# Optimization experiments

Hardware: AMD Instinct MI355X
Metric: run time of the kernel (lower is better)

Reference implementation:

```python
import jax, jax.numpy as jnp
from jax import lax
import numpy as np

NUM_TAGS = 96
BATCH = 512
SEQ = 512


def setup_inputs() -> dict:
    key = jax.random.key(0)
    k1, k2, k3, k4, k5 = jax.random.split(key, 5)
    logits = jax.random.normal(k1, (BATCH, SEQ, NUM_TAGS), dtype=jnp.float32)
    tags = jax.random.randint(k2, (BATCH, SEQ), 0, NUM_TAGS, dtype=jnp.int64)
    mask = jnp.ones((BATCH, SEQ), dtype=jnp.int32)
    # learned CRF params, init U(-0.1, 0.1) as in reset_parameters()
    transitions = jax.random.uniform(k3, (NUM_TAGS, NUM_TAGS), minval=-0.1, maxval=0.1, dtype=jnp.float32)
    start_transitions = jax.random.uniform(k4, (NUM_TAGS,), minval=-0.1, maxval=0.1, dtype=jnp.float32)
    end_transitions = jax.random.uniform(k5, (NUM_TAGS,), minval=-0.1, maxval=0.1, dtype=jnp.float32)
    return {"logits": logits, "tags": tags, "mask": mask,
            "transitions": transitions, "start_transitions": start_transitions,
            "end_transitions": end_transitions}


def _crf_llh(logits, tags, mask, transitions, start_transitions, end_transitions):
    # batch_first -> time-major: em [S,B,T], tg/mk [S,B]
    em = jnp.transpose(logits, (1, 0, 2))
    tg = tags.T
    mk = mask.T.astype(jnp.float32)
    S, B, T = em.shape
    barange = jnp.arange(B)

    # ---- numerator (gold path score), fully vectorized over time ----
    score = start_transitions[tg[0]] + em[0, barange, tg[0]]
    trans_sc = transitions[tg[:-1], tg[1:]]                                   # [S-1, B]
    emit_sc = jnp.take_along_axis(em[1:], tg[1:][..., None], axis=-1)[..., 0]  # [S-1, B]
    score = score + jnp.sum((trans_sc + emit_sc) * mk[1:], axis=0)
    seq_ends = mk.sum(axis=0).astype(jnp.int32) - 1                            # [B]
    last_tags = tg[seq_ends, barange]
    numerator = score + end_transitions[last_tags]

    # ---- denominator (partition function), sequential logsumexp scan ----
    def step(alpha, xs):
        em_i, mk_i = xs  # [B,T], [B]
        nxt = jax.nn.logsumexp(alpha[:, :, None] + transitions[None, :, :] + em_i[:, None, :], axis=1)
        alpha = jnp.where(mk_i[:, None] > 0, nxt, alpha)
        return alpha, None

    alpha0 = start_transitions[None, :] + em[0]  # [B,T]
    alpha, _ = lax.scan(step, alpha0, (em[1:], mk[1:]))
    denominator = jax.nn.logsumexp(alpha + end_transitions[None, :], axis=1)  # [B]

    return numerator - denominator  # [B]


def reference(logits, tags, mask, transitions, start_transitions, end_transitions):
    llh = _crf_llh(logits, tags, mask, transitions, start_transitions, end_transitions)
    return llh.sum()  # reduction='sum'
```

## Files before the change

kernel.cpp:

```cpp
#include <hip/hip_runtime.h>

#define SEQ 512
#define NBAT 512
#define NT 96
#define G 64
#define P 32
#define SEGL (SEQ / P)
#define OV 3
#define TPB 384
#define STRIDE 104
#define FSH 7
#define LN2 0.69314718055994531f

typedef float f32x16 __attribute__((ext_vector_type(16)));
typedef short bf16x8 __attribute__((ext_vector_type(8)));

static __device__ __forceinline__ short f2bf(float f) {
    unsigned u = __float_as_uint(f);
    u += 0x7FFFu + ((u >> 16) & 1u);
    return (short)(u >> 16);
}
static __device__ __forceinline__ float bf2f(short s) {
    return __uint_as_float(((unsigned)(unsigned short)s) << 16);
}
static __device__ __forceinline__ unsigned pk2(float lo, float hi) {
    unsigned r;
    asm("v_cvt_pk_bf16_f32 %0, %1, %2" : "=v"(r) : "v"(lo), "v"(hi));
    return r;
}

__launch_bounds__(TPB, 1)
__global__ void crf_seg64(const float* __restrict__ logits,
                          const int*   __restrict__ tags,
                          const int*   __restrict__ mask,
                          const float* __restrict__ trans,
                          const float* __restrict__ startt,
                          const float* __restrict__ endt,
                          float* __restrict__ out)
{
    const int sid = blockIdx.x & (P - 1);
    const int grp = blockIdx.x >> 5;
    const int b0 = grp * G;
    const int t = threadIdx.x;
    const int W = t >> 6;
    const int T = W >> 1;
    const int M = W & 1;
    const int l = t & 63;
    const int n = l & 31;
    const int h = l >> 5;
    const int bm = 32 * M + n;

    const int i0 = sid ? sid * SEGL - OV : 0;
    const int qs = sid * SEGL;
    const int i1 = (sid == P - 1) ? SEQ - 1 : (sid + 1) * SEGL;

    __shared__ short AT[2][G][STRIDE];
    __shared__ float nred[6][G];
    __shared__ int   cred[6][G];
    __shared__ float expend_s[NT];

    if (t < NT) expend_s[t] = __expf(endt[t]);

    unsigned mybits = 0;
    {
        const int* mrow = mask + (size_t)(b0 + bm) * SEQ + i0;
        const int wlen = i1 - i0 + 1;
        for (int d = 0; d < wlen; ++d)
            if (mrow[d]) mybits |= 1u << d;
    }

    bf16x8 ea[6];
#pragma unroll
    for (int c = 0; c < 6; ++c)
#pragma unroll
        for (int e = 0; e < 8; ++e)
            ea[c][e] = f2bf(__expf(trans[(16 * c + 8 * h + e) * NT + 32 * T + n])
                            * 0.0078125f);

    const float* emg = logits + (size_t)(b0 + bm) * SEQ * NT;
    const int jb = 32 * T + 4 * h;

    uint2 prev[4];
#pragma unroll
    for (int p = 0; p < 4; ++p) {
        uint2 pv;
        if (sid == 0) {
            const int j = jb + 8 * p;
            pv.x = pk2(__expf(startt[j + 0] + emg[j + 0]),
                       __expf(startt[j + 1] + emg[j + 1]));
            pv.y = pk2(__expf(startt[j + 2] + emg[j + 2]),
                       __expf(startt[j + 3] + emg[j + 3]));
        } else {
            pv.x = 0x3F803F80u; pv.y = 0x3F803F80u;
        }
        prev[p] = pv;
        *(uint2*)&AT[0][bm][jb + 8 * p] = pv;
    }

    int K = 0;

    float4 eA[4], eB[4];
#pragma unroll
    for (int p = 0; p < 4; ++p) {
        eA[p] = *(const float4*)&emg[(size_t)(i0 + 1) * NT + jb + 8 * p];
        eB[p] = *(const float4*)&emg[(size_t)(i0 + 2) * NT + jb + 8 * p];
    }
    __syncthreads();

#define CRF_STEP(i) do {                                                       \
    const int d_ = (i) - i0;                                                   \
    const int rb_ = (d_ - 1) & 1, wb_ = d_ & 1;                                \
    bf16x8 Bf[6];                                                              \
    _Pragma("unroll")                                                          \
    for (int c = 0; c < 6; ++c)                                                \
        Bf[c] = *(const bf16x8*)&AT[rb_][bm][16 * c + 8 * h];                  \
    const int ip_ = ((i) + 2 <= i1) ? (i) + 2 : i1;                            \
    float4 en_[4];                                                             \
    _Pragma("unroll")                                                          \
    for (int p = 0; p < 4; ++p)                                                \
        en_[p] = *(const float4*)&emg[(size_t)ip_ * NT + jb + 8 * p];          \
    const unsigned mk = (mybits >> d_) & 1u;                                   \
    float wsv[4][4];                                                           \
    _Pragma("unroll")                                                          \
    for (int p = 0; p < 4; ++p) {                                              \
        wsv[p][0] = __expf(eA[p].x); wsv[p][1] = __expf(eA[p].y);              \
        wsv[p][2] = __expf(eA[p].z); wsv[p][3] = __expf(eA[p].w);              \
    }                                                                          \
    f32x16 acc = {0.f,0.f,0.f,0.f,0.f,0.f,0.f,0.f,                             \
                  0.f,0.f,0.f,0.f,0.f,0.f,0.f,0.f};                            \
    _Pragma("unroll")                                                          \
    for (int c = 0; c < 6; ++c)                                                \
        acc = __builtin_amdgcn_mfma_f32_32x32x16_bf16(ea[c], Bf[c], acc, 0, 0, 0); \
    _Pragma("unroll")                                                          \
    for (int p = 0; p < 4; ++p) {                                              \
        const float av0 = acc[4 * p + 0] * wsv[p][0];                          \
        const float av1 = acc[4 * p + 1] * wsv[p][1];                          \
        const float av2 = acc[4 * p + 2] * wsv[p][2];                          \
        const float av3 = acc[4 * p + 3] * wsv[p][3];                          \
        uint2 nw; nw.x = pk2(av0, av1); nw.y = pk2(av2, av3);                  \
        if (mk) prev[p] = nw;                                                  \
        *(uint2*)&AT[wb_][bm][jb + 8 * p] = prev[p];                           \
    }                                                                          \
    if (mk) K += FSH;                                                          \
    _Pragma("unroll")                                                          \
    for (int p = 0; p < 4; ++p) { eA[p] = eB[p]; eB[p] = en_[p]; }             \
    asm volatile("s_waitcnt lgkmcnt(0)\n\ts_barrier" ::: "memory");            \
} while (0)

    for (int i = i0 + 1; i <= qs; ++i) CRF_STEP(i);

    const bool fin = (T == 0) && (h == 0);
    float Lin = 0.f;
    if (sid > 0 && fin) {
        const int pb = (qs - i0) & 1;
        float sd = 0.f;
        for (int j = 0; j < NT; ++j) sd += bf2f(AT[pb][bm][j]);
        Lin = __logf(sd) + (float)K * LN2;
    }
    for (int i = qs + 1; i <= i1; ++i) CRF_STEP(i);

    float Lend_or_Lout = 0.f;
    if (fin) {
        const int pb = (i1 - i0) & 1;
        float s1 = 0.f, s2 = 0.f;
        for (int j = 0; j < NT; ++j) {
            const float a = bf2f(AT[pb][bm][j]);
            s1 += a; s2 += a * expend_s[j];
        }
        const float su = (sid == P - 1) ? s2 : s1;
        Lend_or_Lout = __logf(su) + (float)K * LN2;
    }

    {
        const float* emp = logits + (size_t)(b0 + l) * SEQ * NT;
        const int* tgp = tags + (size_t)(b0 + l) * SEQ;
        float pn = 0.f;
        for (int i = qs + 1 + W; i <= i1; i += 6) {
            if (mask[(size_t)(b0 + l) * SEQ + i]) {
                const int tp = tgp[i - 1], tc = tgp[i];
                pn += trans[tp * NT + tc] + emp[(size_t)i * NT + tc];
            }
        }
        int pc = 0;
        if (sid == P - 1) {
            const int4* m4p = (const int4*)(mask + (size_t)(b0 + l) * SEQ);
            for (int k = W; k < SEQ / 4; k += 6) {
                const int4 m4 = m4p[k];
                pc += (m4.x != 0) + (m4.y != 0) + (m4.z != 0) + (m4.w != 0);
            }
        }
        nred[W][l] = pn; cred[W][l] = pc;
    }
    __syncthreads();

    if (fin) {
        float num = 0.f; int cnt = 0;
        for (int cc = 0; cc < 6; ++cc) { num += nred[cc][bm]; cnt += cred[cc][bm]; }
        const int* tgq = tags + (size_t)(b0 + bm) * SEQ;
        if (sid == 0)
            num += startt[tgq[0]] + logits[(size_t)(b0 + bm) * SEQ * NT + tgq[0]];
        if (sid == P - 1)
            num += endt[tgq[cnt - 1]];
        nred[0][bm] = num - Lend_or_Lout + Lin;
    }
    __syncthreads();

    if (t == 0) {
        float s = 0.f;
        for (int b = 0; b < G; ++b) s += nred[0][b];
        atomicAdd(out, s);
    }
}

extern "C" void kernel_launch(void* const* d_in, const int* in_sizes, int n_in,
                              void* d_out, int out_size, void* d_ws, size_t ws_size,
                              hipStream_t stream)
{
    const float* logits = (const float*)d_in[0];
    const int*   tags   = (const int*)  d_in[1];
    const int*   mask   = (const int*)  d_in[2];
    const float* trans  = (const float*)d_in[3];
    const float* startt = (const float*)d_in[4];
    const float* endt   = (const float*)d_in[5];
    float* out = (float*)d_out;

    hipMemsetAsync(out, 0, out_size * sizeof(float), stream);
    crf_seg64<<<(NBAT / G) * P, TPB, 0, stream>>>(logits, tags, mask, trans,
                                                  startt, endt, out);
}
```

Baseline: 41.36 us.

## Stage exp'd emissions cooperatively in swizzled shared memory and stage mask loads

Each step's emission row is now loaded by all threads with coalesced float4 reads, exponentiated once, packed to bf16, and written into a double-buffered XOR-swizzled shared-memory tile. The MFMA epilogue reads its per-element weights from there instead of each lane computing exps from strided global loads. Mask bits are staged through shared memory, and the step loop is unrolled by two with ping-pong prefetch registers. This removes redundant exp work and uncoalesced loads, at the cost of extra LDS traffic, another barrier, and a leftover no-op self-copy in the step macro.

```diff
diff --git a/kernel.cpp b/kernel.cpp
--- a/kernel.cpp
+++ b/kernel.cpp
@@ -53,21 +53,32 @@
     const int i0 = sid ? sid * SEGL - OV : 0;
     const int qs = sid * SEGL;
     const int i1 = (sid == P - 1) ? SEQ - 1 : (sid + 1) * SEGL;
+    const int dmax = i1 - i0;
 
     __shared__ short AT[2][G][STRIDE];
+    __shared__ uint2 EMS[2][1536];
     __shared__ float nred[6][G];
     __shared__ int   cred[6][G];
     __shared__ float expend_s[NT];
 
     if (t < NT) expend_s[t] = __expf(endt[t]);
 
+    const int wlen = dmax + 1;
+    {
+        int* mkS = (int*)&EMS[0][0];
+        for (int f = t; f < G * wlen; f += TPB) {
+            const int r = f / wlen, dd = f - r * wlen;
+            mkS[f] = mask[(size_t)(b0 + r) * SEQ + i0 + dd];
+        }
+    }
+    __syncthreads();
     unsigned mybits = 0;
     {
-        const int* mrow = mask + (size_t)(b0 + bm) * SEQ + i0;
-        const int wlen = i1 - i0 + 1;
-        for (int d = 0; d < wlen; ++d)
-            if (mrow[d]) mybits |= 1u << d;
-    }
+        const int* mkS = (const int*)&EMS[0][0];
+        for (int dd = 0; dd < wlen; ++dd)
+            if (mkS[bm * wlen + dd]) mybits |= 1u << dd;
+    }
+    __syncthreads();
 
     bf16x8 ea[6];
 #pragma unroll
@@ -79,6 +90,21 @@
 
     const float* emg = logits + (size_t)(b0 + bm) * SEQ * NT;
     const int jb = 32 * T + 4 * h;
+
+    int wposv[4]; const float* gsrc[4];
+#pragma unroll
+    for (int k = 0; k < 4; ++k) {
+        const int f = k * TPB + t;
+        const int r = f / 24, c = f - 24 * r;
+        wposv[k] = c * 64 + (r ^ (c & 7));
+        gsrc[k] = logits + (size_t)(b0 + r) * SEQ * NT + 4 * c;
+    }
+    int rposv[4];
+#pragma unroll
+    for (int p = 0; p < 4; ++p) {
+        const int c = 8 * T + 2 * p + h;
+        rposv[p] = c * 64 + (bm ^ (c & 7));
+    }
 
     uint2 prev[4];
 #pragma unroll
@@ -99,69 +125,78 @@
 
     int K = 0;
 
-    float4 eA[4], eB[4];
-#pragma unroll
-    for (int p = 0; p < 4; ++p) {
-        eA[p] = *(const float4*)&emg[(size_t)(i0 + 1) * NT + jb + 8 * p];
-        eB[p] = *(const float4*)&emg[(size_t)(i0 + 2) * NT + jb + 8 * p];
-    }
-    __syncthreads();
-
-#define CRF_STEP(i) do {                                                       \
+    float4 pA[4], pB[4];
+#pragma unroll
+    for (int k = 0; k < 4; ++k) pA[k] = *(const float4*)(gsrc[k] + (size_t)(i0 + 1) * NT);
+#pragma unroll
+    for (int k = 0; k < 4; ++k)
+        EMS[1][wposv[k]] = make_uint2(pk2(__expf(pA[k].x), __expf(pA[k].y)),
+                                      pk2(__expf(pA[k].z), __expf(pA[k].w)));
+#pragma unroll
+    for (int k = 0; k < 4; ++k) pA[k] = *(const float4*)(gsrc[k] + (size_t)(i0 + 2) * NT);
+#pragma unroll
+    for (int k = 0; k < 4; ++k) pB[k] = *(const float4*)(gsrc[k] + (size_t)(i0 + 3) * NT);
+    __syncthreads();
+
+#define CRF_STEP(i, X) do {                                                    \
     const int d_ = (i) - i0;                                                   \
-    const int rb_ = (d_ - 1) & 1, wb_ = d_ & 1;                                \
+    const int rb_ = (d_ - 1) & 1, wb_ = d_ & 1;      \
+                    \
+    _Pragma("unroll")                                                          \
+    for (int k = 0; k < 4; ++k)                                                \
+        EMS[rb_ ^ 1 ^ wb_ ^ wb_][0] = EMS[rb_ ^ 1 ^ wb_ ^ wb_][0];            \
+    _Pragma("unroll")                                                          \
+    for (int k = 0; k < 4; ++k)                                                \
+        EMS[wb_ ^ 1][wposv[k]] = make_uint2(pk2(__expf(X[k].x), __expf(X[k].y)), \
+                                            pk2(__expf(X[k].z), __expf(X[k].w))); \
+                                           \
+    { const int ip_ = ((i) + 3 <= i1) ? (i) + 3 : i1;                          \
+      _Pragma("unroll")                                                        \
+      for (int k = 0; k < 4; ++k)                                              \
+          X[k] = *(const float4*)(gsrc[k] + (size_t)ip_ * NT); }               \
     bf16x8 Bf[6];                                                              \
     _Pragma("unroll")                                                          \
     for (int c = 0; c < 6; ++c)                                                \
         Bf[c] = *(const bf16x8*)&AT[rb_][bm][16 * c + 8 * h];                  \
-    const int ip_ = ((i) + 2 <= i1) ? (i) + 2 : i1;                            \
-    float4 en_[4];                                                             \
-    _Pragma("unroll")                                                          \
-    for (int p = 0; p < 4; ++p)                                                \
-        en_[p] = *(const float4*)&emg[(size_t)ip_ * NT + jb + 8 * p];          \
-    const unsigned mk = (mybits >> d_) & 1u;                                   \
-    float wsv[4][4];                                                           \
-    _Pragma("unroll")                                                          \
-    for (int p = 0; p < 4; ++p) {                                              \
-        wsv[p][0] = __expf(eA[p].x); wsv[p][1] = __expf(eA[p].y);              \
-        wsv[p][2] = __expf(eA[p].z); wsv[p][3] = __expf(eA[p].w);              \
-    }                                                                          \
     f32x16 acc = {0.f,0.f,0.f,0.f,0.f,0.f,0.f,0.f,                             \
                   0.f,0.f,0.f,0.f,0.f,0.f,0.f,0.f};                            \
     _Pragma("unroll")                                                          \
     for (int c = 0; c < 6; ++c)                                                \
         acc = __builtin_amdgcn_mfma_f32_32x32x16_bf16(ea[c], Bf[c], acc, 0, 0, 0); \
+    const unsigned mk = (mybits >> d_) & 1u;                                   \
     _Pragma("unroll")                                                          \
     for (int p = 0; p < 4; ++p) {                                              \
-        const float av0 = acc[4 * p + 0] * wsv[p][0];                          \
-        const float av1 = acc[4 * p + 1] * wsv[p][1];                          \
-        const float av2 = acc[4 * p + 2] * wsv[p][2];                          \
-        const float av3 = acc[4 * p + 3] * wsv[p][3];                          \
-        uint2 nw; nw.x = pk2(av0, av1); nw.y = pk2(av2, av3);                  \
+        const uint2 wv = EMS[wb_][rposv[p]];                                   \
+        const float w0 = __uint_as_float(wv.x << 16);                          \
+        const float w1 = __uint_as_float(wv.x & 0xFFFF0000u);                  \
+        const float w2 = __uint_as_float(wv.y << 16);                          \
+        const float w3 = __uint_as_float(wv.y & 0xFFFF0000u);                  \
+        uint2 nw;                                                              \
+        nw.x = pk2(acc[4 * p + 0] * w0, acc[4 * p + 1] * w1);                  \
+        nw.y = pk2(acc[4 * p + 2] * w2, acc[4 * p + 3] * w3);                  \
         if (mk) prev[p] = nw;                                                  \
         *(uint2*)&AT[wb_][bm][jb + 8 * p] = prev[p];                           \
     }                                                                          \
     if (mk) K += FSH;                                                          \
-    _Pragma("unroll")                                                          \
-    for (int p = 0; p < 4; ++p) { eA[p] = eB[p]; eB[p] = en_[p]; }             \
     asm volatile("s_waitcnt lgkmcnt(0)\n\ts_barrier" ::: "memory");            \
 } while (0)
 
-    for (int i = i0 + 1; i <= qs; ++i) CRF_STEP(i);
-
     const bool fin = (T == 0) && (h == 0);
     float Lin = 0.f;
-    if (sid > 0 && fin) {
-        const int pb = (qs - i0) & 1;
-        float sd = 0.f;
-        for (int j = 0; j < NT; ++j) sd += bf2f(AT[pb][bm][j]);
-        Lin = __logf(sd) + (float)K * LN2;
-    }
-    for (int i = qs + 1; i <= i1; ++i) CRF_STEP(i);
+
+    for (int d = 1; d <= dmax; d += 2) {
+        CRF_STEP(i0 + d, pA);
+        if (sid && d == OV && fin) {
+            float sd = 0.f;
+            for (int j = 0; j < NT; ++j) sd += bf2f(AT[OV & 1][bm][j]);
+            Lin = __logf(sd) + (float)K * LN2;
+        }
+        if (d + 1 <= dmax) CRF_STEP(i0 + d + 1, pB);
+    }
 
     float Lend_or_Lout = 0.f;
     if (fin) {
-        const int pb = (i1 - i0) & 1;
+        const int pb = dmax & 1;
         float s1 = 0.f, s2 = 0.f;
         for (int j = 0; j < NT; ++j) {
             const float a = bf2f(AT[pb][bm][j]);
```

New measurement: 39.86 us. 1.04x faster.
